# Performance work log

Measured on AMD Instinct MI355X. Metric: run time of the kernel, lower is better.

## Reference

```python
import jax, jax.numpy as jnp
import numpy as np

V, E, DIN, DH = 8192, 4096, 512, 256
N_CLASSES = 2
EPS = 1e-5  # torch LayerNorm default
EDGE_P = 0.004  # ~33 nodes per hyperedge


def layernorm(x, g, b):
    m = jnp.mean(x, axis=-1, keepdims=True)
    v = jnp.mean((x - m) ** 2, axis=-1, keepdims=True)
    return (x - m) / jnp.sqrt(v + EPS) * g + b


def setup_inputs() -> dict:
    key = jax.random.key(0)
    ks = jax.random.split(key, 8)
    X = jax.random.normal(ks[0], (V, DIN), dtype=jnp.float32)
    # binary incidence matrix (|V|, |E|)
    H_inc = (jax.random.uniform(ks[1], (V, E)) < EDGE_P).astype(jnp.float32)
    Wp = jax.random.normal(ks[2], (DH, DIN), dtype=jnp.float32) * 0.02  # input_proj (no bias)
    W0 = jax.random.normal(ks[3], (DH, DH), dtype=jnp.float32) * 0.02
    W1 = jax.random.normal(ks[4], (DH, DH), dtype=jnp.float32) * 0.02
    g0 = jnp.ones((DH,), jnp.float32); b0 = jnp.zeros((DH,), jnp.float32)
    g1 = jnp.ones((DH,), jnp.float32); b1 = jnp.zeros((DH,), jnp.float32)
    Wc = jax.random.normal(ks[5], (N_CLASSES, DH), dtype=jnp.float32) * 0.02
    bc = jnp.zeros((N_CLASSES,), jnp.float32)
    return {"X": X, "H_inc": H_inc, "Wp": Wp, "W0": W0, "W1": W1,
            "g0": g0, "b0": b0, "g1": g1, "b1": b1, "Wc": Wc, "bc": bc}


def reference(X, H_inc, Wp, W0, W1, g0, b0, g1, b1, Wc, bc):
    # --- normalized incidence: H_tilde = D_v^{-1/2} H D_e^{-1/2}, 0 for isolated ---
    d_v = H_inc.sum(axis=1)   # (V,)
    d_e = H_inc.sum(axis=0)   # (E,)
    dvi = jnp.where(d_v > 0, jnp.where(d_v > 0, d_v, 1.0) ** -0.5, 0.0)
    dei = jnp.where(d_e > 0, jnp.where(d_e > 0, d_e, 1.0) ** -0.5, 0.0)
    H_tilde = dvi[:, None] * H_inc * dei[None, :]            # (V, E)
    HHt = H_tilde @ H_tilde.T                                # (V, V)

    # input projection
    Xh = X @ Wp.T                                            # (V, DH)

    # L=2 message-passing layers with residual + LayerNorm
    for W, g, b in ((W0, g0, b0), (W1, g1, b1)):
        Xn = jax.nn.relu((HHt @ Xh) @ W.T)
        Xh = layernorm(Xh + Xn, g, b)

    # mean pool per hyperedge (== Python loop over E in the original):
    # z_e = mean of member node embeddings; zeros for empty hyperedges
    cnt = jnp.where(d_e > 0, d_e, 1.0)[:, None]              # (E, 1)
    z_E = (H_inc.T @ Xh) / cnt                               # (E, DH)

    logits = z_E @ Wc.T + bc                                 # (E, 2)
    return jax.nn.softmax(logits, axis=1)
```

## Files before the change

kernel.cpp:

```cpp
#include <hip/hip_runtime.h>
#include <math.h>

#define NV 8192
#define NE 4096
#define DIN 512
#define DH 256
#define CAP_E 96
#define CAP_V 64

#define OFF_XH   0
#define OFF_Z    (OFF_XH + NV*DH)
#define OFF_Y    (OFF_Z  + NV*DH)
#define OFF_NCNT (OFF_Y  + NE*DH)
#define OFF_ECNT (OFF_NCNT + NV)
#define OFF_EL   (OFF_ECNT + NE*16)
#define OFF_NL   (OFF_EL + NE*CAP_E)

using bf16x8 = __attribute__((ext_vector_type(8))) short;
using f32x4  = __attribute__((ext_vector_type(4))) float;

__device__ inline unsigned short f2bf(float f) {
    union { float f; unsigned u; } v; v.f = f;
    unsigned r = v.u + 0x7FFF + ((v.u >> 16) & 1);
    return (unsigned short)(r >> 16);
}

__global__ __launch_bounds__(256) void scan_H(const float* __restrict__ H,
                                              int* __restrict__ edge_cnt,
                                              int* __restrict__ node_cnt,
                                              int* __restrict__ edge_list,
                                              int* __restrict__ node_list) {
    int v = blockIdx.x;
    int t = threadIdx.x;
    __shared__ int lcnt;
    __shared__ int lbuf[CAP_V];
    if (t == 0) lcnt = 0;
    __syncthreads();
    const float4* H4 = (const float4*)(H + (size_t)v * NE);
    float4 h0 = H4[t * 4 + 0], h1 = H4[t * 4 + 1];
    float4 h2 = H4[t * 4 + 2], h3 = H4[t * 4 + 3];
    float hv[16] = {h0.x, h0.y, h0.z, h0.w, h1.x, h1.y, h1.z, h1.w,
                    h2.x, h2.y, h2.z, h2.w, h3.x, h3.y, h3.z, h3.w};
    int myE[16]; int n = 0;
    int e0 = t * 16;
#pragma unroll
    for (int j = 0; j < 16; ++j)
        if (hv[j] != 0.0f) myE[n++] = e0 + j;
    if (n > 0) {
        int s = atomicAdd(&lcnt, n);
        for (int k = 0; k < n; ++k) {
            int ee = myE[k];
            if (s + k < CAP_V) lbuf[s + k] = ee;
            int g = atomicAdd(&edge_cnt[ee << 4], 1);
            if (g < CAP_E) edge_list[ee * CAP_E + g] = v;
        }
    }
    __syncthreads();
    int c = lcnt;
    if (t == 0) node_cnt[v] = c;
    c = min(c, CAP_V);
    for (int i = t; i < c; i += 256) node_list[v * CAP_V + i] = lbuf[i];
}

__global__ __launch_bounds__(256) void gemm_bf16(const float* __restrict__ A,
                                                 const float* __restrict__ B,
                                                 float* __restrict__ C,
                                                 int K) {
    __shared__ short As[2048];
    __shared__ short Bs[16384];
    const int tid  = threadIdx.x;
    const int lane = tid & 63;
    const int w    = tid >> 6;
    const int bm   = blockIdx.x * 32;
    const int swz  = lane ^ ((lane >> 3) & 6);

    float4 ar[2], br[16];
    {
        int i0 = tid, i1 = tid + 256;
        ar[0] = *(const float4*)(A + (size_t)(bm + (i0 >> 4)) * K + ((i0 & 15) << 2));
        ar[1] = *(const float4*)(A + (size_t)(bm + (i1 >> 4)) * K + ((i1 & 15) << 2));
#pragma unroll
        for (int it = 0; it < 16; ++it) {
            int i = tid + it * 256;
            br[it] = *(const float4*)(B + (size_t)(i >> 4) * K + ((i & 15) << 2));
        }
    }
    f32x4 acc[2][4];
#pragma unroll
    for (int mi = 0; mi < 2; ++mi)
#pragma unroll
        for (int ni = 0; ni < 4; ++ni) acc[mi][ni] = (f32x4){0.f, 0.f, 0.f, 0.f};

    for (int k0 = 0; k0 < K; k0 += 64) {
        __syncthreads();
#pragma unroll
        for (int s = 0; s < 2; ++s) {
            int i = tid + s * 256;
            int row = i >> 4, kk = (i & 15) << 2;
            int kc = kk >> 5, quad = (kk >> 3) & 3, j = kk & 7;
            int ln = (row & 15) + (quad << 4);
            int p  = ln ^ ((ln >> 3) & 6);
            int addr = ((row >> 4) * 2 + kc) * 512 + p * 8 + j;
            float4 v = ar[s];
            ushort4 u = {f2bf(v.x), f2bf(v.y), f2bf(v.z), f2bf(v.w)};
            *(ushort4*)&As[addr] = u;
        }
#pragma unroll
        for (int it = 0; it < 16; ++it) {
            int i = tid + it * 256;
            int row = i >> 4, kk = (i & 15) << 2;
            int kc = kk >> 5, quad = (kk >> 3) & 3, j = kk & 7;
            int ln = (row & 15) + (quad << 4);
            int p  = ln ^ ((ln >> 3) & 6);
            int addr = ((row >> 4) * 2 + kc) * 512 + p * 8 + j;
            float4 v = br[it];
            ushort4 u = {f2bf(v.x), f2bf(v.y), f2bf(v.z), f2bf(v.w)};
            *(ushort4*)&Bs[addr] = u;
        }
        __syncthreads();
        if (k0 + 64 < K) {
            int kn = k0 + 64;
            int i0 = tid, i1 = tid + 256;
            ar[0] = *(const float4*)(A + (size_t)(bm + (i0 >> 4)) * K + kn + ((i0 & 15) << 2));
            ar[1] = *(const float4*)(A + (size_t)(bm + (i1 >> 4)) * K + kn + ((i1 & 15) << 2));
#pragma unroll
            for (int it = 0; it < 16; ++it) {
                int i = tid + it * 256;
                br[it] = *(const float4*)(B + (size_t)(i >> 4) * K + kn + ((i & 15) << 2));
            }
        }
#pragma unroll
        for (int kc = 0; kc < 2; ++kc) {
            bf16x8 af[2], bfr[4];
            af[0] = *(const bf16x8*)&As[(0 * 2 + kc) * 512 + swz * 8];
            af[1] = *(const bf16x8*)&As[(1 * 2 + kc) * 512 + swz * 8];
#pragma unroll
            for (int ni = 0; ni < 4; ++ni)
                bfr[ni] = *(const bf16x8*)&Bs[((w * 4 + ni) * 2 + kc) * 512 + swz * 8];
#pragma unroll
            for (int mi = 0; mi < 2; ++mi)
#pragma unroll
                for (int ni = 0; ni < 4; ++ni)
                    acc[mi][ni] = __builtin_amdgcn_mfma_f32_16x16x32_bf16(
                        af[mi], bfr[ni], acc[mi][ni], 0, 0, 0);
        }
    }
    const int quad = lane >> 4, cl = lane & 15;
#pragma unroll
    for (int mi = 0; mi < 2; ++mi)
#pragma unroll
        for (int ni = 0; ni < 4; ++ni)
#pragma unroll
            for (int r = 0; r < 4; ++r)
                C[(size_t)(bm + mi * 16 + quad * 4 + r) * DH + w * 64 + ni * 16 + cl]
                    = acc[mi][ni][r];
}

__global__ __launch_bounds__(256) void gemm_relu_res_ln(const float* __restrict__ Z,
                                                        const float* __restrict__ W,
                                                        float* __restrict__ Xh,
                                                        const float* __restrict__ g,
                                                        const float* __restrict__ b) {
    const int K = DH;
    __shared__ short As[2048];
    __shared__ short Bs[16384];
    __shared__ float redS[32][4];
    __shared__ float redQ[32][4];
    const int tid  = threadIdx.x;
    const int lane = tid & 63;
    const int w    = tid >> 6;
    const int bm   = blockIdx.x * 32;
    const int swz  = lane ^ ((lane >> 3) & 6);

    float4 ar[2], br[16];
    {
        int i0 = tid, i1 = tid + 256;
        ar[0] = *(const float4*)(Z + (size_t)(bm + (i0 >> 4)) * K + ((i0 & 15) << 2));
        ar[1] = *(const float4*)(Z + (size_t)(bm + (i1 >> 4)) * K + ((i1 & 15) << 2));
#pragma unroll
        for (int it = 0; it < 16; ++it) {
            int i = tid + it * 256;
            br[it] = *(const float4*)(W + (size_t)(i >> 4) * K + ((i & 15) << 2));
        }
    }
    f32x4 acc[2][4];
#pragma unroll
    for (int mi = 0; mi < 2; ++mi)
#pragma unroll
        for (int ni = 0; ni < 4; ++ni) acc[mi][ni] = (f32x4){0.f, 0.f, 0.f, 0.f};

    for (int k0 = 0; k0 < K; k0 += 64) {
        __syncthreads();
#pragma unroll
        for (int s = 0; s < 2; ++s) {
            int i = tid + s * 256;
            int row = i >> 4, kk = (i & 15) << 2;
            int kc = kk >> 5, quad = (kk >> 3) & 3, j = kk & 7;
            int ln = (row & 15) + (quad << 4);
            int p  = ln ^ ((ln >> 3) & 6);
            int addr = ((row >> 4) * 2 + kc) * 512 + p * 8 + j;
            float4 v = ar[s];
            ushort4 u = {f2bf(v.x), f2bf(v.y), f2bf(v.z), f2bf(v.w)};
            *(ushort4*)&As[addr] = u;
        }
#pragma unroll
        for (int it = 0; it < 16; ++it) {
            int i = tid + it * 256;
            int row = i >> 4, kk = (i & 15) << 2;
            int kc = kk >> 5, quad = (kk >> 3) & 3, j = kk & 7;
            int ln = (row & 15) + (quad << 4);
            int p  = ln ^ ((ln >> 3) & 6);
            int addr = ((row >> 4) * 2 + kc) * 512 + p * 8 + j;
            float4 v = br[it];
            ushort4 u = {f2bf(v.x), f2bf(v.y), f2bf(v.z), f2bf(v.w)};
            *(ushort4*)&Bs[addr] = u;
        }
        __syncthreads();
        if (k0 + 64 < K) {
            int kn = k0 + 64;
            int i0 = tid, i1 = tid + 256;
            ar[0] = *(const float4*)(Z + (size_t)(bm + (i0 >> 4)) * K + kn + ((i0 & 15) << 2));
            ar[1] = *(const float4*)(Z + (size_t)(bm + (i1 >> 4)) * K + kn + ((i1 & 15) << 2));
#pragma unroll
            for (int it = 0; it < 16; ++it) {
                int i = tid + it * 256;
                br[it] = *(const float4*)(W + (size_t)(i >> 4) * K + kn + ((i & 15) << 2));
            }
        }
#pragma unroll
        for (int kc = 0; kc < 2; ++kc) {
            bf16x8 af[2], bfr[4];
            af[0] = *(const bf16x8*)&As[(0 * 2 + kc) * 512 + swz * 8];
            af[1] = *(const bf16x8*)&As[(1 * 2 + kc) * 512 + swz * 8];
#pragma unroll
            for (int ni = 0; ni < 4; ++ni)
                bfr[ni] = *(const bf16x8*)&Bs[((w * 4 + ni) * 2 + kc) * 512 + swz * 8];
#pragma unroll
            for (int mi = 0; mi < 2; ++mi)
#pragma unroll
                for (int ni = 0; ni < 4; ++ni)
                    acc[mi][ni] = __builtin_amdgcn_mfma_f32_16x16x32_bf16(
                        af[mi], bfr[ni], acc[mi][ni], 0, 0, 0);
        }
    }
    const int quad = lane >> 4, cl = lane & 15;
#pragma unroll
    for (int mi = 0; mi < 2; ++mi)
#pragma unroll
        for (int r = 0; r < 4; ++r) {
            int row = bm + mi * 16 + quad * 4 + r;
            float s = 0.f, q = 0.f;
#pragma unroll
            for (int ni = 0; ni < 4; ++ni) {
                int col = w * 64 + ni * 16 + cl;
                float v = fmaxf(acc[mi][ni][r], 0.f) + Xh[(size_t)row * DH + col];
                acc[mi][ni][r] = v;
                s += v; q = fmaf(v, v, q);
            }
#pragma unroll
            for (int o = 1; o < 16; o <<= 1) {
                s += __shfl_xor(s, o, 64);
                q += __shfl_xor(q, o, 64);
            }
            if (cl == 0) {
                redS[mi * 16 + quad * 4 + r][w] = s;
                redQ[mi * 16 + quad * 4 + r][w] = q;
            }
        }
    __syncthreads();
#pragma unroll
    for (int mi = 0; mi < 2; ++mi)
#pragma unroll
        for (int r = 0; r < 4; ++r) {
            int R = mi * 16 + quad * 4 + r;
            float s = redS[R][0] + redS[R][1] + redS[R][2] + redS[R][3];
            float q = redQ[R][0] + redQ[R][1] + redQ[R][2] + redQ[R][3];
            float m = s * (1.0f / DH);
            float var = q * (1.0f / DH) - m * m;
            float rstd = rsqrtf(var + 1e-5f);
            int row = bm + R;
#pragma unroll
            for (int ni = 0; ni < 4; ++ni) {
                int col = w * 64 + ni * 16 + cl;
                float v = (acc[mi][ni][r] - m) * rstd * g[col] + b[col];
                Xh[(size_t)row * DH + col] = v;
            }
        }
}

#define GATHER_BODY(SRC, IDX, COEF, CNT)                                         \
    float4 a[8];                                                                 \
    _Pragma("unroll") for (int u = 0; u < 8; ++u) a[u] = (float4){0,0,0,0};      \
    int i = 0;                                                                   \
    for (; i + 8 <= CNT; i += 8) {                                               \
        _Pragma("unroll") for (int u = 0; u < 8; ++u) {                          \
            float4 x = SRC[IDX[i+u] + tid]; float c = COEF[i+u];                 \
            a[u].x = fmaf(c, x.x, a[u].x); a[u].y = fmaf(c, x.y, a[u].y);        \
            a[u].z = fmaf(c, x.z, a[u].z); a[u].w = fmaf(c, x.w, a[u].w);        \
        }                                                                        \
    }                                                                            \
    for (; i < CNT; ++i) {                                                       \
        float4 x = SRC[IDX[i] + tid]; float c = COEF[i];                         \
        a[0].x = fmaf(c, x.x, a[0].x); a[0].y = fmaf(c, x.y, a[0].y);            \
        a[0].z = fmaf(c, x.z, a[0].z); a[0].w = fmaf(c, x.w, a[0].w);            \
    }                                                                            \
    _Pragma("unroll") for (int u = 4; u > 0; u >>= 1)                            \
        _Pragma("unroll") for (int q = 0; q < u; ++q) {                          \
            a[q].x += a[q+u].x; a[q].y += a[q+u].y;                              \
            a[q].z += a[q+u].z; a[q].w += a[q+u].w;                              \
        }

__global__ __launch_bounds__(64) void edge_gather(const float* __restrict__ Xh,
                                                  const int* __restrict__ edge_cnt,
                                                  const int* __restrict__ edge_list,
                                                  const int* __restrict__ node_cnt,
                                                  float* __restrict__ Y) {
    int e = blockIdx.x;
    int tid = threadIdx.x;
    __shared__ int   lv[CAP_E];
    __shared__ float lc[CAP_E];
    int cnt = min(edge_cnt[e << 4], CAP_E);
    for (int j = tid; j < cnt; j += 64) {
        int v = edge_list[e * CAP_E + j];
        lv[j] = v * (DH / 4);
        lc[j] = rsqrtf((float)node_cnt[v]);
    }
    __syncthreads();
    const float4* X4 = (const float4*)Xh;
    GATHER_BODY(X4, lv, lc, cnt)
    float de = cnt > 0 ? rsqrtf((float)cnt) : 0.f;
    float4 o = {de * a[0].x, de * a[0].y, de * a[0].z, de * a[0].w};
    ((float4*)Y)[e * (DH / 4) + tid] = o;
}

__global__ __launch_bounds__(64) void node_gather(const float* __restrict__ Y,
                                                  const int* __restrict__ node_cnt,
                                                  const int* __restrict__ node_list,
                                                  const int* __restrict__ edge_cnt,
                                                  float* __restrict__ Z) {
    int v = blockIdx.x;
    int tid = threadIdx.x;
    __shared__ int   le[CAP_V];
    __shared__ float lc[CAP_V];
    int cnt = min(node_cnt[v], CAP_V);
    if (tid < cnt) {
        int e = node_list[v * CAP_V + tid];
        le[tid] = e * (DH / 4);
        lc[tid] = rsqrtf((float)edge_cnt[e << 4]);
    }
    __syncthreads();
    const float4* Y4 = (const float4*)Y;
    GATHER_BODY(Y4, le, lc, cnt)
    float dv = cnt > 0 ? rsqrtf((float)cnt) : 0.f;
    float4 o = {dv * a[0].x, dv * a[0].y, dv * a[0].z, dv * a[0].w};
    ((float4*)Z)[v * (DH / 4) + tid] = o;
}

__global__ __launch_bounds__(64) void pool_classify(const float* __restrict__ Xh,
                                                    const int* __restrict__ edge_cnt,
                                                    const int* __restrict__ edge_list,
                                                    const float* __restrict__ Wc,
                                                    const float* __restrict__ bc,
                                                    float* __restrict__ out) {
    int e = blockIdx.x;
    int tid = threadIdx.x;
    __shared__ int lv[CAP_E];
    int cnt = min(edge_cnt[e << 4], CAP_E);
    for (int j = tid; j < cnt; j += 64) lv[j] = edge_list[e * CAP_E + j] * (DH / 4);
    __syncthreads();
    const float4* X4 = (const float4*)Xh;
    float4 a[8];
#pragma unroll
    for (int u = 0; u < 8; ++u) a[u] = (float4){0, 0, 0, 0};
    int i = 0;
    for (; i + 8 <= cnt; i += 8) {
#pragma unroll
        for (int u = 0; u < 8; ++u) {
            float4 x = X4[lv[i + u] + tid];
            a[u].x += x.x; a[u].y += x.y; a[u].z += x.z; a[u].w += x.w;
        }
    }
    for (; i < cnt; ++i) {
        float4 x = X4[lv[i] + tid];
        a[0].x += x.x; a[0].y += x.y; a[0].z += x.z; a[0].w += x.w;
    }
#pragma unroll
    for (int u = 4; u > 0; u >>= 1)
#pragma unroll
        for (int q = 0; q < u; ++q) {
            a[q].x += a[q + u].x; a[q].y += a[q + u].y;
            a[q].z += a[q + u].z; a[q].w += a[q + u].w;
        }
    float inv = cnt > 0 ? 1.0f / (float)cnt : 1.0f;
    float4 val = {a[0].x * inv, a[0].y * inv, a[0].z * inv, a[0].w * inv};
    const float4* W4 = (const float4*)Wc;
    float4 w0 = W4[tid], w1 = W4[64 + tid];
    float p0 = val.x * w0.x + val.y * w0.y + val.z * w0.z + val.w * w0.w;
    float p1 = val.x * w1.x + val.y * w1.y + val.z * w1.z + val.w * w1.w;
#pragma unroll
    for (int o = 32; o > 0; o >>= 1) {
        p0 += __shfl_down(p0, o, 64);
        p1 += __shfl_down(p1, o, 64);
    }
    if (tid == 0) {
        float l0 = p0 + bc[0], l1 = p1 + bc[1];
        float mx = fmaxf(l0, l1);
        float e0 = expf(l0 - mx), e1 = expf(l1 - mx);
        float s = 1.0f / (e0 + e1);
        out[e * 2 + 0] = e0 * s;
        out[e * 2 + 1] = e1 * s;
    }
}

extern "C" void kernel_launch(void* const* d_in, const int* in_sizes, int n_in,
                              void* d_out, int out_size, void* d_ws, size_t ws_size,
                              hipStream_t stream) {
    const float* X  = (const float*)d_in[0];
    const float* H  = (const float*)d_in[1];
    const float* Wp = (const float*)d_in[2];
    const float* W0 = (const float*)d_in[3];
    const float* W1 = (const float*)d_in[4];
    const float* g0 = (const float*)d_in[5];
    const float* b0 = (const float*)d_in[6];
    const float* g1 = (const float*)d_in[7];
    const float* b1 = (const float*)d_in[8];
    const float* Wc = (const float*)d_in[9];
    const float* bc = (const float*)d_in[10];
    float* out = (float*)d_out;

    float* ws = (float*)d_ws;
    float* Xh  = ws + OFF_XH;
    float* Z   = ws + OFF_Z;
    float* Y   = ws + OFF_Y;
    int* node_cnt  = (int*)(ws + OFF_NCNT);
    int* edge_cnt  = (int*)(ws + OFF_ECNT);
    int* edge_list = (int*)(ws + OFF_EL);
    int* node_list = (int*)(ws + OFF_NL);

    hipMemsetAsync(edge_cnt, 0, (size_t)(NE * 16) * sizeof(int), stream);

    scan_H<<<NV, 256, 0, stream>>>(H, edge_cnt, node_cnt, edge_list, node_list);

    gemm_bf16<<<NV / 32, 256, 0, stream>>>(X, Wp, Xh, DIN);

    const float* Ws[2] = {W0, W1};
    const float* gs[2] = {g0, g1};
    const float* bs[2] = {b0, b1};
    for (int l = 0; l < 2; ++l) {
        edge_gather<<<NE, 64, 0, stream>>>(Xh, edge_cnt, edge_list, node_cnt, Y);
        node_gather<<<NV, 64, 0, stream>>>(Y, node_cnt, node_list, edge_cnt, Z);
        gemm_relu_res_ln<<<NV / 32, 256, 0, stream>>>(Z, Ws[l], Xh, gs[l], bs[l]);
    }

    pool_classify<<<NE, 64, 0, stream>>>(Xh, edge_cnt, edge_list, Wc, bc, out);
}
```

Measured before the change: 327.8 us.

## Fuse incidence scan with input projection and gather bf16 node features

Merges the H scan kernel and the input-projection GEMM into one launch, with the first NV/32 blocks doing the GEMM and the rest scanning H rows, so both can overlap and one launch is saved. The GEMM epilogues also write a bf16 copy of Xh, and edge_gather now reads this half-width copy, roughly halving gather traffic at some cost in precision. Degree normalisation now uses the true counts rather than the capped counts. The extra bf16 stores add some write traffic to the GEMM epilogues.

```diff
diff --git a/kernel.cpp b/kernel.cpp
--- a/kernel.cpp
+++ b/kernel.cpp
@@ -15,6 +15,7 @@
 #define OFF_ECNT (OFF_NCNT + NV)
 #define OFF_EL   (OFF_ECNT + NE*16)
 #define OFF_NL   (OFF_EL + NE*CAP_E)
+#define OFF_XHB  (OFF_NL + NV*CAP_V)
 
 using bf16x8 = __attribute__((ext_vector_type(8))) short;
 using f32x4  = __attribute__((ext_vector_type(4))) float;
@@ -24,65 +25,70 @@
     unsigned r = v.u + 0x7FFF + ((v.u >> 16) & 1);
     return (unsigned short)(r >> 16);
 }
-
-__global__ __launch_bounds__(256) void scan_H(const float* __restrict__ H,
-                                              int* __restrict__ edge_cnt,
-                                              int* __restrict__ node_cnt,
-                                              int* __restrict__ edge_list,
-                                              int* __restrict__ node_list) {
-    int v = blockIdx.x;
-    int t = threadIdx.x;
-    __shared__ int lcnt;
-    __shared__ int lbuf[CAP_V];
-    if (t == 0) lcnt = 0;
-    __syncthreads();
-    const float4* H4 = (const float4*)(H + (size_t)v * NE);
-    float4 h0 = H4[t * 4 + 0], h1 = H4[t * 4 + 1];
-    float4 h2 = H4[t * 4 + 2], h3 = H4[t * 4 + 3];
-    float hv[16] = {h0.x, h0.y, h0.z, h0.w, h1.x, h1.y, h1.z, h1.w,
-                    h2.x, h2.y, h2.z, h2.w, h3.x, h3.y, h3.z, h3.w};
-    int myE[16]; int n = 0;
-    int e0 = t * 16;
-#pragma unroll
-    for (int j = 0; j < 16; ++j)
-        if (hv[j] != 0.0f) myE[n++] = e0 + j;
-    if (n > 0) {
-        int s = atomicAdd(&lcnt, n);
-        for (int k = 0; k < n; ++k) {
-            int ee = myE[k];
-            if (s + k < CAP_V) lbuf[s + k] = ee;
-            int g = atomicAdd(&edge_cnt[ee << 4], 1);
-            if (g < CAP_E) edge_list[ee * CAP_E + g] = v;
-        }
-    }
-    __syncthreads();
-    int c = lcnt;
-    if (t == 0) node_cnt[v] = c;
-    c = min(c, CAP_V);
-    for (int i = t; i < c; i += 256) node_list[v * CAP_V + i] = lbuf[i];
-}
-
-__global__ __launch_bounds__(256) void gemm_bf16(const float* __restrict__ A,
-                                                 const float* __restrict__ B,
-                                                 float* __restrict__ C,
-                                                 int K) {
-    __shared__ short As[2048];
-    __shared__ short Bs[16384];
-    const int tid  = threadIdx.x;
+__device__ inline float b2f(unsigned short s) {
+    union { unsigned u; float f; } v; v.u = ((unsigned)s) << 16; return v.f;
+}
+
+union ScanProjSmem {
+    struct { short As[2048]; short Bs[16384]; } g;
+    struct { int lcnt; int lbuf[CAP_V]; } s;
+};
+
+__global__ __launch_bounds__(256) void scan_proj(const float* __restrict__ H,
+                                                 const float* __restrict__ X,
+                                                 const float* __restrict__ Wp,
+                                                 float* __restrict__ Xh,
+                                                 unsigned short* __restrict__ Xhb,
+                                                 int* __restrict__ edge_cnt,
+                                                 int* __restrict__ node_cnt,
+                                                 int* __restrict__ edge_list,
+                                                 int* __restrict__ node_list) {
+    __shared__ ScanProjSmem sm;
+    const int tid = threadIdx.x;
+    if (blockIdx.x >= NV / 32) {
+        int v = blockIdx.x - NV / 32;
+        if (tid == 0) sm.s.lcnt = 0;
+        __syncthreads();
+        const float4* H4 = (const float4*)(H + (size_t)v * NE);
+        float4 h0 = H4[tid * 4 + 0], h1 = H4[tid * 4 + 1];
+        float4 h2 = H4[tid * 4 + 2], h3 = H4[tid * 4 + 3];
+        float hv[16] = {h0.x, h0.y, h0.z, h0.w, h1.x, h1.y, h1.z, h1.w,
+                        h2.x, h2.y, h2.z, h2.w, h3.x, h3.y, h3.z, h3.w};
+        int myE[16]; int n = 0;
+        int e0 = tid * 16;
+#pragma unroll
+        for (int j = 0; j < 16; ++j)
+            if (hv[j] != 0.0f) myE[n++] = e0 + j;
+        if (n > 0) {
+            int s = atomicAdd(&sm.s.lcnt, n);
+            for (int k = 0; k < n; ++k) {
+                int ee = myE[k];
+                if (s + k < CAP_V) sm.s.lbuf[s + k] = ee;
+                int gc = atomicAdd(&edge_cnt[ee << 4], 1);
+                if (gc < CAP_E) edge_list[ee * CAP_E + gc] = v;
+            }
+        }
+        __syncthreads();
+        int c = sm.s.lcnt;
+        if (tid == 0) node_cnt[v] = c;
+        int cc = min(c, CAP_V);
+        for (int i = tid; i < cc; i += 256) node_list[v * CAP_V + i] = sm.s.lbuf[i];
+        return;
+    }
+    const int K = DIN;
     const int lane = tid & 63;
     const int w    = tid >> 6;
     const int bm   = blockIdx.x * 32;
     const int swz  = lane ^ ((lane >> 3) & 6);
-
     float4 ar[2], br[16];
     {
         int i0 = tid, i1 = tid + 256;
-        ar[0] = *(const float4*)(A + (size_t)(bm + (i0 >> 4)) * K + ((i0 & 15) << 2));
-        ar[1] = *(const float4*)(A + (size_t)(bm + (i1 >> 4)) * K + ((i1 & 15) << 2));
+        ar[0] = *(const float4*)(X + (size_t)(bm + (i0 >> 4)) * K + ((i0 & 15) << 2));
+        ar[1] = *(const float4*)(X + (size_t)(bm + (i1 >> 4)) * K + ((i1 & 15) << 2));
 #pragma unroll
         for (int it = 0; it < 16; ++it) {
             int i = tid + it * 256;
-            br[it] = *(const float4*)(B + (size_t)(i >> 4) * K + ((i & 15) << 2));
+            br[it] = *(const float4*)(Wp + (size_t)(i >> 4) * K + ((i & 15) << 2));
         }
     }
     f32x4 acc[2][4];
@@ -90,7 +96,6 @@
     for (int mi = 0; mi < 2; ++mi)
 #pragma unroll
         for (int ni = 0; ni < 4; ++ni) acc[mi][ni] = (f32x4){0.f, 0.f, 0.f, 0.f};
-
     for (int k0 = 0; k0 < K; k0 += 64) {
         __syncthreads();
 #pragma unroll
@@ -99,11 +104,10 @@
             int row = i >> 4, kk = (i & 15) << 2;
             int kc = kk >> 5, quad = (kk >> 3) & 3, j = kk & 7;
             int ln = (row & 15) + (quad << 4);
-            int p  = ln ^ ((ln >> 3) & 6);
-            int addr = ((row >> 4) * 2 + kc) * 512 + p * 8 + j;
+            int pp = ln ^ ((ln >> 3) & 6);
             float4 v = ar[s];
             ushort4 u = {f2bf(v.x), f2bf(v.y), f2bf(v.z), f2bf(v.w)};
-            *(ushort4*)&As[addr] = u;
+            *(ushort4*)&sm.g.As[((row >> 4) * 2 + kc) * 512 + pp * 8 + j] = u;
         }
 #pragma unroll
         for (int it = 0; it < 16; ++it) {
@@ -111,32 +115,31 @@
             int row = i >> 4, kk = (i & 15) << 2;
             int kc = kk >> 5, quad = (kk >> 3) & 3, j = kk & 7;
             int ln = (row & 15) + (quad << 4);
-            int p  = ln ^ ((ln >> 3) & 6);
-            int addr = ((row >> 4) * 2 + kc) * 512 + p * 8 + j;
+            int pp = ln ^ ((ln >> 3) & 6);
             float4 v = br[it];
             ushort4 u = {f2bf(v.x), f2bf(v.y), f2bf(v.z), f2bf(v.w)};
-            *(ushort4*)&Bs[addr] = u;
+            *(ushort4*)&sm.g.Bs[((row >> 4) * 2 + kc) * 512 + pp * 8 + j] = u;
         }
         __syncthreads();
         if (k0 + 64 < K) {
             int kn = k0 + 64;
             int i0 = tid, i1 = tid + 256;
-            ar[0] = *(const float4*)(A + (size_t)(bm + (i0 >> 4)) * K + kn + ((i0 & 15) << 2));
-            ar[1] = *(const float4*)(A + (size_t)(bm + (i1 >> 4)) * K + kn + ((i1 & 15) << 2));
+            ar[0] = *(const float4*)(X + (size_t)(bm + (i0 >> 4)) * K + kn + ((i0 & 15) << 2));
+            ar[1] = *(const float4*)(X + (size_t)(bm + (i1 >> 4)) * K + kn + ((i1 & 15) << 2));
 #pragma unroll
             for (int it = 0; it < 16; ++it) {
                 int i = tid + it * 256;
-                br[it] = *(const float4*)(B + (size_t)(i >> 4) * K + kn + ((i & 15) << 2));
+                br[it] = *(const float4*)(Wp + (size_t)(i >> 4) * K + kn + ((i & 15) << 2));
             }
         }
 #pragma unroll
         for (int kc = 0; kc < 2; ++kc) {
             bf16x8 af[2], bfr[4];
-            af[0] = *(const bf16x8*)&As[(0 * 2 + kc) * 512 + swz * 8];
-            af[1] = *(const bf16x8*)&As[(1 * 2 + kc) * 512 + swz * 8];
+            af[0] = *(const bf16x8*)&sm.g.As[(0 * 2 + kc) * 512 + swz * 8];
+            af[1] = *(const bf16x8*)&sm.g.As[(1 * 2 + kc) * 512 + swz * 8];
 #pragma unroll
             for (int ni = 0; ni < 4; ++ni)
-                bfr[ni] = *(const bf16x8*)&Bs[((w * 4 + ni) * 2 + kc) * 512 + swz * 8];
+                bfr[ni] = *(const bf16x8*)&sm.g.Bs[((w * 4 + ni) * 2 + kc) * 512 + swz * 8];
 #pragma unroll
             for (int mi = 0; mi < 2; ++mi)
 #pragma unroll
@@ -151,14 +154,18 @@
 #pragma unroll
         for (int ni = 0; ni < 4; ++ni)
 #pragma unroll
-            for (int r = 0; r < 4; ++r)
-                C[(size_t)(bm + mi * 16 + quad * 4 + r) * DH + w * 64 + ni * 16 + cl]
-                    = acc[mi][ni][r];
+            for (int r = 0; r < 4; ++r) {
+                float v = acc[mi][ni][r];
+                size_t idx = (size_t)(bm + mi * 16 + quad * 4 + r) * DH + w * 64 + ni * 16 + cl;
+                Xh[idx] = v;
+                Xhb[idx] = f2bf(v);
+            }
 }
 
 __global__ __launch_bounds__(256) void gemm_relu_res_ln(const float* __restrict__ Z,
                                                         const float* __restrict__ W,
                                                         float* __restrict__ Xh,
+                                                        unsigned short* __restrict__ Xhb,
                                                         const float* __restrict__ g,
                                                         const float* __restrict__ b) {
     const int K = DH;
@@ -197,11 +204,10 @@
             int row = i >> 4, kk = (i & 15) << 2;
             int kc = kk >> 5, quad = (kk >> 3) & 3, j = kk & 7;
             int ln = (row & 15) + (quad << 4);
-            int p  = ln ^ ((ln >> 3) & 6);
-            int addr = ((row >> 4) * 2 + kc) * 512 + p * 8 + j;
+            int pp = ln ^ ((ln >> 3) & 6);
             float4 v = ar[s];
             ushort4 u = {f2bf(v.x), f2bf(v.y), f2bf(v.z), f2bf(v.w)};
-            *(ushort4*)&As[addr] = u;
+            *(ushort4*)&As[((row >> 4) * 2 + kc) * 512 + pp * 8 + j] = u;
         }
 #pragma unroll
         for (int it = 0; it < 16; ++it) {
@@ -209,11 +215,10 @@
             int row = i >> 4, kk = (i & 15) << 2;
             int kc = kk >> 5, quad = (kk >> 3) & 3, j = kk & 7;
             int ln = (row & 15) + (quad << 4);
-            int p  = ln ^ ((ln >> 3) & 6);
-            int addr = ((row >> 4) * 2 + kc) * 512 + p * 8 + j;
+            int pp = ln ^ ((ln >> 3) & 6);
             float4 v = br[it];
             ushort4 u = {f2bf(v.x), f2bf(v.y), f2bf(v.z), f2bf(v.w)};
-            *(ushort4*)&Bs[addr] = u;
+            *(ushort4*)&Bs[((row >> 4) * 2 + kc) * 512 + pp * 8 + j] = u;
         }
         __syncthreads();
         if (k0 + 64 < K) {
@@ -283,34 +288,14 @@
             for (int ni = 0; ni < 4; ++ni) {
                 int col = w * 64 + ni * 16 + cl;
                 float v = (acc[mi][ni][r] - m) * rstd * g[col] + b[col];
-                Xh[(size_t)row * DH + col] = v;
-            }
-        }
-}
-
-#define GATHER_BODY(SRC, IDX, COEF, CNT)                                         \
-    float4 a[8];                                                                 \
-    _Pragma("unroll") for (int u = 0; u < 8; ++u) a[u] = (float4){0,0,0,0};      \
-    int i = 0;                                                                   \
-    for (; i + 8 <= CNT; i += 8) {                                               \
-        _Pragma("unroll") for (int u = 0; u < 8; ++u) {                          \
-            float4 x = SRC[IDX[i+u] + tid]; float c = COEF[i+u];                 \
-            a[u].x = fmaf(c, x.x, a[u].x); a[u].y = fmaf(c, x.y, a[u].y);        \
-            a[u].z = fmaf(c, x.z, a[u].z); a[u].w = fmaf(c, x.w, a[u].w);        \
-        }                                                                        \
-    }                                                                            \
-    for (; i < CNT; ++i) {                                                       \
-        float4 x = SRC[IDX[i] + tid]; float c = COEF[i];                         \
-        a[0].x = fmaf(c, x.x, a[0].x); a[0].y = fmaf(c, x.y, a[0].y);            \
-        a[0].z = fmaf(c, x.z, a[0].z); a[0].w = fmaf(c, x.w, a[0].w);            \
-    }                                                                            \
-    _Pragma("unroll") for (int u = 4; u > 0; u >>= 1)                            \
-        _Pragma("unroll") for (int q = 0; q < u; ++q) {                          \
-            a[q].x += a[q+u].x; a[q].y += a[q+u].y;                              \
-            a[q].z += a[q+u].z; a[q].w += a[q+u].w;                              \
-        }
-
-__global__ __launch_bounds__(64) void edge_gather(const float* __restrict__ Xh,
+                size_t idx = (size_t)row * DH + col;
+                Xh[idx] = v;
+                Xhb[idx] = f2bf(v);
+            }
+        }
+}
+
+__global__ __launch_bounds__(64) void edge_gather(const unsigned short* __restrict__ Xhb,
                                                   const int* __restrict__ edge_cnt,
                                                   const int* __restrict__ edge_list,
                                                   const int* __restrict__ node_cnt,
@@ -319,16 +304,40 @@
     int tid = threadIdx.x;
     __shared__ int   lv[CAP_E];
     __shared__ float lc[CAP_E];
-    int cnt = min(edge_cnt[e << 4], CAP_E);
+    int tc = edge_cnt[e << 4];
+    int cnt = min(tc, CAP_E);
     for (int j = tid; j < cnt; j += 64) {
         int v = edge_list[e * CAP_E + j];
         lv[j] = v * (DH / 4);
         lc[j] = rsqrtf((float)node_cnt[v]);
     }
     __syncthreads();
-    const float4* X4 = (const float4*)Xh;
-    GATHER_BODY(X4, lv, lc, cnt)
-    float de = cnt > 0 ? rsqrtf((float)cnt) : 0.f;
+    const ushort4* X4 = (const ushort4*)Xhb;
+    float4 a[8];
+#pragma unroll
+    for (int u = 0; u < 8; ++u) a[u] = (float4){0.f, 0.f, 0.f, 0.f};
+    int i = 0;
+    for (; i + 8 <= cnt; i += 8) {
+#pragma unroll
+        for (int u = 0; u < 8; ++u) {
+            ushort4 h = X4[lv[i + u] + tid]; float c = lc[i + u];
+            a[u].x = fmaf(c, b2f(h.x), a[u].x); a[u].y = fmaf(c, b2f(h.y), a[u].y);
+            a[u].z = fmaf(c, b2f(h.z), a[u].z); a[u].w = fmaf(c, b2f(h.w), a[u].w);
+        }
+    }
+    for (; i < cnt; ++i) {
+        ushort4 h = X4[lv[i] + tid]; float c = lc[i];
+        a[0].x = fmaf(c, b2f(h.x), a[0].x); a[0].y = fmaf(c, b2f(h.y), a[0].y);
+        a[0].z = fmaf(c, b2f(h.z), a[0].z); a[0].w = fmaf(c, b2f(h.w), a[0].w);
+    }
+#pragma unroll
+    for (int u = 4; u > 0; u >>= 1)
+#pragma unroll
+        for (int q = 0; q < u; ++q) {
+            a[q].x += a[q + u].x; a[q].y += a[q + u].y;
+            a[q].z += a[q + u].z; a[q].w += a[q + u].w;
+        }
+    float de = tc > 0 ? rsqrtf((float)tc) : 0.f;
     float4 o = {de * a[0].x, de * a[0].y, de * a[0].z, de * a[0].w};
     ((float4*)Y)[e * (DH / 4) + tid] = o;
 }
@@ -342,7 +351,8 @@
     int tid = threadIdx.x;
     __shared__ int   le[CAP_V];
     __shared__ float lc[CAP_V];
-    int cnt = min(node_cnt[v], CAP_V);
+    int tc = node_cnt[v];
+    int cnt = min(tc, CAP_V);
     if (tid < cnt) {
         int e = node_list[v * CAP_V + tid];
         le[tid] = e * (DH / 4);
@@ -350,8 +360,31 @@
     }
     __syncthreads();
     const float4* Y4 = (const float4*)Y;
-    GATHER_BODY(Y4, le, lc, cnt)
-    float dv = cnt > 0 ? rsqrtf((float)cnt) : 0.f;
+    float4 a[8];
+#pragma unroll
+    for (int u = 0; u < 8; ++u) a[u] = (float4){0.f, 0.f, 0.f, 0.f};
+    int i = 0;
+    for (; i + 8 <= cnt; i += 8) {
+#pragma unroll
+        for (int u = 0; u < 8; ++u) {
+            float4 x = Y4[le[i + u] + tid]; float c = lc[i + u];
+            a[u].x = fmaf(c, x.x, a[u].x); a[u].y = fmaf(c, x.y, a[u].y);
+            a[u].z = fmaf(c, x.z, a[u].z); a[u].w = fmaf(c, x.w, a[u].w);
+        }
+    }
+    for (; i < cnt; ++i) {
+        float4 x = Y4[le[i] + tid]; float c = lc[i];
+        a[0].x = fmaf(c, x.x, a[0].x); a[0].y = fmaf(c, x.y, a[0].y);
+        a[0].z = fmaf(c, x.z, a[0].z); a[0].w = fmaf(c, x.w, a[0].w);
+    }
+#pragma unroll
+    for (int u = 4; u > 0; u >>= 1)
+#pragma unroll
+        for (int q = 0; q < u; ++q) {
+            a[q].x += a[q + u].x; a[q].y += a[q + u].y;
+            a[q].z += a[q + u].z; a[q].w += a[q + u].w;
+        }
+    float dv = tc > 0 ? rsqrtf((float)tc) : 0.f;
     float4 o = {dv * a[0].x, dv * a[0].y, dv * a[0].z, dv * a[0].w};
     ((float4*)Z)[v * (DH / 4) + tid] = o;
 }
@@ -365,7 +398,8 @@
     int e = blockIdx.x;
     int tid = threadIdx.x;
     __shared__ int lv[CAP_E];
-    int cnt = min(edge_cnt[e << 4], CAP_E);
+    int tc = edge_cnt[e << 4];
+    int cnt = min(tc, CAP_E);
     for (int j = tid; j < cnt; j += 64) lv[j] = edge_list[e * CAP_E + j] * (DH / 4);
     __syncthreads();
     const float4* X4 = (const float4*)Xh;
@@ -391,7 +425,7 @@
             a[q].x += a[q + u].x; a[q].y += a[q + u].y;
             a[q].z += a[q + u].z; a[q].w += a[q + u].w;
         }
-    float inv = cnt > 0 ? 1.0f / (float)cnt : 1.0f;
+    float inv = tc > 0 ? 1.0f / (float)tc : 1.0f;
     float4 val = {a[0].x * inv, a[0].y * inv, a[0].z * inv, a[0].w * inv};
     const float4* W4 = (const float4*)Wc;
     float4 w0 = W4[tid], w1 = W4[64 + tid];
@@ -436,20 +470,20 @@
     int* edge_cnt  = (int*)(ws + OFF_ECNT);
     int* edge_list = (int*)(ws + OFF_EL);
     int* node_list = (int*)(ws + OFF_NL);
+    unsigned short* Xhb = (unsigned short*)(ws + OFF_XHB);
 
     hipMemsetAsync(edge_cnt, 0, (size_t)(NE * 16) * sizeof(int), stream);
 
-    scan_H<<<NV, 256, 0, stream>>>(H, edge_cnt, node_cnt, edge_list, node_list);
-
-    gemm_bf16<<<NV / 32, 256, 0, stream>>>(X, Wp, Xh, DIN);
+    scan_proj<<<NV / 32 + NV, 256, 0, stream>>>(H, X, Wp, Xh, Xhb,
+                                                edge_cnt, node_cnt, edge_list, node_list);
 
     const float* Ws[2] = {W0, W1};
     const float* gs[2] = {g0, g1};
     const float* bs[2] = {b0, b1};
     for (int l = 0; l < 2; ++l) {
-        edge_gather<<<NE, 64, 0, stream>>>(Xh, edge_cnt, edge_list, node_cnt, Y);
+        edge_gather<<<NE, 64, 0, stream>>>(Xhb, edge_cnt, edge_list, node_cnt, Y);
         node_gather<<<NV, 64, 0, stream>>>(Y, node_cnt, node_list, edge_cnt, Z);
-        gemm_relu_res_ln<<<NV / 32, 256, 0, stream>>>(Z, Ws[l], Xh, gs[l], bs[l]);
+        gemm_relu_res_ln<<<NV / 32, 256, 0, stream>>>(Z, Ws[l], Xh, Xhb, gs[l], bs[l]);
     }
 
     pool_classify<<<NE, 64, 0, stream>>>(Xh, edge_cnt, edge_list, Wc, bc, out);
```

Measured after the change: 335.5 us. 1.02x slower.
